# Optimization experiments

Hardware: AMD Instinct MI355X
Metric: run time of the kernel (lower is better)

## Reference

```python
import jax, jax.numpy as jnp
import numpy as np

NUM_HEADS = 16

def setup_inputs() -> dict:
    key = jax.random.key(0)
    ks = jax.random.split(key, 3)
    B, S, D = 2, 2048, 1024
    x = jax.random.normal(ks[0], (B, S, D), dtype=jnp.float32)
    # xavier-uniform style scaling for weights
    Wqkv = jax.random.normal(ks[1], (3 * D, D), dtype=jnp.float32) * (1.0 / jnp.sqrt(D))
    bqkv = jnp.zeros((3 * D,), dtype=jnp.float32)
    Wo = jax.random.normal(ks[2], (D, D), dtype=jnp.float32) * (1.0 / jnp.sqrt(D))
    bo = jnp.zeros((D,), dtype=jnp.float32)
    return {"x": x, "Wqkv": Wqkv, "bqkv": bqkv, "Wo": Wo, "bo": bo}

def reference(x, Wqkv, bqkv, Wo, bo):
    B, S, D = x.shape
    H = NUM_HEADS
    hd = D // H
    # qkv projection (torch Linear: x @ W.T + b)
    qkv = x @ Wqkv.T + bqkv                      # [B, S, 3D]
    qkv = qkv.reshape(B, S, H, 3 * hd).transpose(0, 2, 1, 3)  # [B, H, S, 3hd]
    q, k, v = jnp.split(qkv, 3, axis=-1)         # each [B, H, S, hd]
    scale = 1.0 / jnp.sqrt(jnp.asarray(hd, dtype=x.dtype))
    logits = jnp.einsum('bhqd,bhkd->bhqk', q, k) * scale  # [B, H, S, S]
    attn = jax.nn.softmax(logits, axis=-1)
    vals = jnp.einsum('bhqk,bhkd->bhqd', attn, v)         # [B, H, S, hd]
    vals = vals.transpose(0, 2, 1, 3).reshape(B, S, D)
    return vals @ Wo.T + bo
```

## Files before the change

### kernel.cpp

```cpp
#include <hip/hip_runtime.h>


typedef short short8 __attribute__((ext_vector_type(8)));
typedef unsigned short ushort8v __attribute__((ext_vector_type(8)));
typedef unsigned short ushort4v __attribute__((ext_vector_type(4)));
typedef float floatx4 __attribute__((ext_vector_type(4)));

#define S_LEN 2048
#define D_MODEL 1024
#define N_HEADS 16
#define HEAD_DIM 64

#define EXP2F(x) __builtin_amdgcn_exp2f(x)

__device__ inline float bf2f(unsigned int u16) {
    union { unsigned int i; float f; } v; v.i = u16 << 16; return v.f;
}
__device__ inline unsigned short f2b(float f) {
    union { float f; unsigned int u; } v; v.f = f;
    return (unsigned short)((v.u + 0x7FFFu + ((v.u >> 16) & 1u)) >> 16);
}
__device__ inline unsigned int fbits(float f) {
    union { float f; unsigned int u; } v; v.f = f; return v.u;
}
__device__ inline unsigned int pack_bf2(float lo, float hi) {
    return __byte_perm(fbits(lo) + 0x8000u, fbits(hi) + 0x8000u, 0x7632);
}

__device__ inline void gld_lds16(const unsigned short* g, unsigned short* lds) {
    __builtin_amdgcn_global_load_lds(
        (const __attribute__((address_space(1))) void*)g,
        (__attribute__((address_space(3))) void*)lds, 16, 0, 0);
}

__global__ __launch_bounds__(256)
void cvt3(const float* __restrict__ s0, const float* __restrict__ s1,
          const float* __restrict__ s2,
          unsigned short* __restrict__ d0, unsigned short* __restrict__ d1,
          unsigned short* __restrict__ d2,
          int n0, int n1, int n2) {
    const int total = n0 + n1 + n2;
    for (int g = blockIdx.x * blockDim.x + threadIdx.x; g < total;
         g += gridDim.x * blockDim.x) {
        const float* s; unsigned short* d; int l;
        if (g < n0)            { s = s0; d = d0; l = g; }
        else if (g < n0 + n1)  { s = s1; d = d1; l = g - n0; }
        else                   { s = s2; d = d2; l = g - n0 - n1; }
        const float4* sp = (const float4*)s + (size_t)l * 2;
        float4 f0 = sp[0], f1 = sp[1];
        ushort8v o;
        o[0] = f2b(f0.x); o[1] = f2b(f0.y); o[2] = f2b(f0.z); o[3] = f2b(f0.w);
        o[4] = f2b(f1.x); o[5] = f2b(f1.y); o[6] = f2b(f1.z); o[7] = f2b(f1.w);
        *(ushort8v*)(d + (size_t)l * 8) = o;
    }
}

__device__ inline void gemm_core(const unsigned short* __restrict__ A,
                                 const unsigned short* __restrict__ W,
                                 int m0, int n0, int K,
                                 unsigned short* As, unsigned short* Bs,
                                 floatx4 acc[4][4]) {
    const int tid  = threadIdx.x;
    const int lane = tid & 63;
    const int wave = tid >> 6;
    const int wm = wave >> 1, wn = wave & 1;
    const int r = lane & 15, q = lane >> 4;

    const int grow = wave * 32 + (lane >> 3);
    const int gcol = (lane & 7) * 8;

    for (int k0 = 0; k0 < K; k0 += 64) {
        __syncthreads();
#pragma unroll
        for (int j = 0; j < 4; j++) {
            gld_lds16(A + (size_t)(m0 + grow + j * 8) * K + k0 + gcol,
                      As + wave * 2048 + j * 512);
            gld_lds16(W + (size_t)(n0 + grow + j * 8) * K + k0 + gcol,
                      Bs + wave * 2048 + j * 512);
        }
        __builtin_amdgcn_s_waitcnt(0);
        __syncthreads();
#pragma unroll
        for (int kk = 0; kk < 64; kk += 32) {
            short8 aF[4], bF[4];
#pragma unroll
            for (int t = 0; t < 4; t++)
                aF[t] = *(const short8*)(As + (wm * 64 + t * 16 + r) * 64 + kk + q * 8);
#pragma unroll
            for (int t = 0; t < 4; t++)
                bF[t] = *(const short8*)(Bs + (wn * 64 + t * 16 + r) * 64 + kk + q * 8);
#pragma unroll
            for (int i = 0; i < 4; i++)
#pragma unroll
                for (int j = 0; j < 4; j++)
                    acc[i][j] = __builtin_amdgcn_mfma_f32_16x16x32_bf16(aF[i], bF[j], acc[i][j], 0, 0, 0);
        }
    }
}

__device__ inline void stage_h(const unsigned short* __restrict__ g, int ldk,
                               unsigned short* lds, int wave, int lane) {
    const int lr  = lane >> 3;
    const int csw = ((lane & 7) ^ lr) * 8;
    const int rw  = wave * 8 + lr;
    gld_lds16(g + (size_t)rw * ldk + csw,        lds + wave * 512);
    gld_lds16(g + (size_t)(rw + 64) * ldk + csw, lds + 4096 + wave * 512);
}

#define QLDB(pBx) do {                                                         \
    _Pragma("unroll")                                                          \
    for (int nj = 0; nj < 4; ++nj) {                                           \
        bF[nj][0] = *(const short8*)((pBx) + nj * 1024 + co0);                 \
        bF[nj][1] = *(const short8*)((pBx) + nj * 1024 + co1);                 \
    }                                                                          \
} while (0)

#define QPHASE(pAx, mq, ...) do {                                              \
    short8 aF[2][2];                                                           \
    _Pragma("unroll")                                                          \
    for (int m2 = 0; m2 < 2; ++m2) {                                           \
        aF[m2][0] = *(const short8*)((pAx) + ((mq) * 2 + m2) * 1024 + co0);    \
        aF[m2][1] = *(const short8*)((pAx) + ((mq) * 2 + m2) * 1024 + co1);    \
    }                                                                          \
    __VA_ARGS__;                                                               \
    __builtin_amdgcn_s_barrier();                                              \
    __builtin_amdgcn_s_setprio(1);                                             \
    _Pragma("unroll")                                                          \
    for (int kk = 0; kk < 2; ++kk)                                             \
        _Pragma("unroll")                                                      \
        for (int m2 = 0; m2 < 2; ++m2)                                         \
            _Pragma("unroll")                                                  \
            for (int nj = 0; nj < 4; ++nj)                                     \
                acc[(mq) * 2 + m2][nj] = __builtin_amdgcn_mfma_f32_16x16x32_bf16( \
                    aF[m2][kk], bF[nj][kk], acc[(mq) * 2 + m2][nj], 0, 0, 0);  \
    __builtin_amdgcn_s_setprio(0);                                             \
    __builtin_amdgcn_s_barrier();                                              \
} while (0)

#define WAIT_VM4() asm volatile("s_waitcnt vmcnt(4)" ::: "memory")
#define WAIT_VM0() asm volatile("s_waitcnt vmcnt(0)" ::: "memory")

__global__ __launch_bounds__(512, 2)
void qkv_gemm(const unsigned short* __restrict__ x,
              const unsigned short* __restrict__ Wqkv,
              const float* __restrict__ bqkv,
              unsigned short* __restrict__ Qb,
              unsigned short* __restrict__ Kb,
              unsigned short* __restrict__ Vb) {
    __shared__ unsigned short AS[2][16384];
    __shared__ unsigned short BS[2][16384];

    const int tid  = threadIdx.x;
    const int lane = tid & 63;
    const int wave = tid >> 6;
    const int wm = wave >> 2;
    const int wn = wave & 3;
    const int r  = lane & 15, q2 = lane >> 4;
    const int K  = D_MODEL;

    const int idx = blockIdx.x;
    const int swz = (idx & 7) * 24 + (idx >> 3);
    const int mb = swz & 15, nb = swz >> 4;
    const int m0 = mb * 256, n0 = nb * 256;

    const unsigned short* Abase = x    + (size_t)m0 * K;
    const unsigned short* Bbase = Wqkv + (size_t)n0 * K;

    const int co0 = ((q2 ^ (r & 7)) * 8);
    const int co1 = (((q2 + 4) ^ (r & 7)) * 8);
    const unsigned short* pA0 = &AS[0][(wm * 128 + r) * 64];
    const unsigned short* pA1 = &AS[1][(wm * 128 + r) * 64];
    const unsigned short* pB0 = &BS[0][(wn * 64 + r) * 64];
    const unsigned short* pB1 = &BS[1][(wn * 64 + r) * 64];

    floatx4 acc[8][4] = {};
    short8 bF[4][2];

    stage_h(Abase,                K, &AS[0][0],    wave, lane);
    stage_h(Abase + 128 * K,      K, &AS[0][8192], wave, lane);
    stage_h(Bbase,                K, &BS[0][0],    wave, lane);
    stage_h(Bbase + 128 * K,      K, &BS[0][8192], wave, lane);
    stage_h(Bbase + 64,           K, &BS[1][0],    wave, lane);
    stage_h(Bbase + 128 * K + 64, K, &BS[1][8192], wave, lane);
    WAIT_VM4();
    __builtin_amdgcn_s_barrier();

    for (int i = 0; i < 8; ++i) {
        const bool more = (i < 7);
        const int kA1 = i * 128 + 64;
        const int kT2 = i * 128 + 128;
        const int kT3 = i * 128 + 192;

        QLDB(pB0);
        QPHASE(pA0, 0, {
            stage_h(Abase + kA1,           K, &AS[1][0],    wave, lane);
            stage_h(Abase + 128 * K + kA1, K, &AS[1][8192], wave, lane);
        });
        QPHASE(pA0, 1, {
            if (more) stage_h(Bbase + kT2, K, &BS[0][0], wave, lane);
        });
        QPHASE(pA0, 2, {
            if (more) stage_h(Bbase + 128 * K + kT2, K, &BS[0][8192], wave, lane);
        });
        QPHASE(pA0, 3, {
            if (more) { WAIT_VM4(); } else { WAIT_VM0(); }
        });
        QLDB(pB1);
        QPHASE(pA1, 0, {
            if (more) {
                stage_h(Abase + kT2,           K, &AS[0][0],    wave, lane);
                stage_h(Abase + 128 * K + kT2, K, &AS[0][8192], wave, lane);
            }
        });
        QPHASE(pA1, 1, {
            if (more) stage_h(Bbase + kT3, K, &BS[1][0], wave, lane);
        });
        QPHASE(pA1, 2, {
            if (more) stage_h(Bbase + 128 * K + kT3, K, &BS[1][8192], wave, lane);
        });
        QPHASE(pA1, 3, {
            if (more) { WAIT_VM4(); }
        });
    }

#pragma unroll
    for (int mi = 0; mi < 8; mi++) {
#pragma unroll
        for (int nj = 0; nj < 4; nj++) {
            int n = n0 + wn * 64 + nj * 16 + r;
            int h = n / 192;
            int rem = n % 192;
            int typ = rem >> 6;
            int d = rem & 63;
            float bv = bqkv[n];
            int m = m0 + wm * 128 + mi * 16 + q2 * 4;
            int b = m >> 11, s = m & 2047;
            if (typ == 2) {
                ushort4v pk;
#pragma unroll
                for (int rg = 0; rg < 4; rg++) pk[rg] = f2b(acc[mi][nj][rg] + bv);
                *(ushort4v*)(Vb + ((size_t)((b * N_HEADS + h) * HEAD_DIM + d)) * S_LEN + s) = pk;
            } else {
                unsigned short* dst = (typ == 0) ? Qb : Kb;
                float sc = (typ == 0) ? 0.180336880f : 1.0f;
#pragma unroll
                for (int rg = 0; rg < 4; rg++)
                    dst[(((size_t)(b * N_HEADS + h)) * S_LEN + s + rg) * HEAD_DIM + d] =
                        f2b((acc[mi][nj][rg] + bv) * sc);
            }
        }
    }
}

__global__ __launch_bounds__(256)
void out_gemm(const unsigned short* __restrict__ vals,
              const unsigned short* __restrict__ Wo,
              const float* __restrict__ bo,
              float* __restrict__ out) {
    __shared__ unsigned short As[128 * 64];
    __shared__ unsigned short Bs[128 * 64];
    const int lane = threadIdx.x & 63;
    const int wave = threadIdx.x >> 6;
    const int wm = wave >> 1, wn = wave & 1;
    const int r = lane & 15, q = lane >> 4;
    const int m0 = blockIdx.y * 128;
    const int n0 = blockIdx.x * 128;

    floatx4 acc[4][4] = {};
    gemm_core(vals, Wo, m0, n0, D_MODEL, As, Bs, acc);

#pragma unroll
    for (int i = 0; i < 4; i++) {
#pragma unroll
        for (int j = 0; j < 4; j++) {
            int n = n0 + wn * 64 + j * 16 + r;
            float bv = bo[n];
#pragma unroll
            for (int rg = 0; rg < 4; rg++) {
                int m = m0 + wm * 64 + i * 16 + q * 4 + rg;
                out[(size_t)m * D_MODEL + n] = acc[i][j][rg] + bv;
            }
        }
    }
}

__global__ __launch_bounds__(256, 2)
void attn_kernel(const unsigned short* __restrict__ Qb,
                 const unsigned short* __restrict__ Kb,
                 const unsigned short* __restrict__ Vg,
                 unsigned short* __restrict__ vals) {
    __shared__ unsigned short QPs[128 * 64];
    __shared__ unsigned short Ks[2 * 64 * 64];
    __shared__ unsigned short Vts[2 * 64 * 64];

    const int tid = threadIdx.x;
    const int lane = tid & 63;
    const int wave = tid >> 6;
    const int r = lane & 15, q2 = lane >> 4;
    const int r7 = r & 7;
    const int w32 = wave * 32;

    const int idx  = blockIdx.x;
    const int xcd  = idx & 7;
    const int slot = idx >> 3;
    const int bh   = (xcd << 2) | (slot >> 4);
    const int q0   = (slot & 15) * 128;
    const int b = bh >> 4, h = bh & 15;

    const unsigned short* Qp = Qb + (size_t)bh * S_LEN * HEAD_DIM;
    const unsigned short* Kp = Kb + (size_t)bh * S_LEN * HEAD_DIM;
    const unsigned short* Vp = Vg + (size_t)bh * HEAD_DIM * S_LEN;

    const int srow = lane >> 3;
    const int scol = ((lane & 7) ^ srow) * 8;

    {
        const int qrow = tid >> 1;
        const int c0 = (tid & 1) * 4;
#pragma unroll
        for (int cc = 0; cc < 4; cc++) {
            int cb = c0 + cc;
            const uint4* gq = (const uint4*)(Qp + (size_t)(q0 + qrow) * HEAD_DIM + cb * 8);
            *(uint4*)(QPs + qrow * 64 + ((cb ^ (qrow & 7)) * 8)) = *gq;
        }
#pragma unroll
        for (int j = 0; j < 16; j += 8) {
            gld_lds16(Kp + (size_t)(wave * 16 + j + srow) * HEAD_DIM + scol,
                      Ks + (wave * 16 + j) * 64);
            gld_lds16(Vp + (size_t)(wave * 16 + j + srow) * S_LEN + scol,
                      Vts + (wave * 16 + j) * 64);
        }
    }
    __builtin_amdgcn_s_waitcnt(0);
    __syncthreads();

    short8 qf[2][2];
#pragma unroll
    for (int nt = 0; nt < 2; nt++)
#pragma unroll
        for (int ks = 0; ks < 2; ks++) {
            int cb = ks * 4 + q2;
            qf[nt][ks] = *(const short8*)(QPs + (w32 + nt * 16 + r) * 64 + ((cb ^ r7) * 8));
        }

    float l_part[2] = {0.f, 0.f};
    floatx4 o_acc[2][4] = {};
    int cur = 0;

    for (int kt = 0; kt < S_LEN; kt += 64) {
        const int more = (kt + 64 < S_LEN);
        if (more) {
            const int nxt = (cur ^ 1) * 4096;
#pragma unroll
            for (int j = 0; j < 16; j += 8) {
                gld_lds16(Kp + (size_t)(kt + 64 + wave * 16 + j + srow) * HEAD_DIM + scol,
                          Ks + nxt + (wave * 16 + j) * 64);
                gld_lds16(Vp + (size_t)(wave * 16 + j + srow) * S_LEN + kt + 64 + scol,
                          Vts + nxt + (wave * 16 + j) * 64);
            }
        }
        const int co = cur * 4096;

        floatx4 sp[4][2] = {};
#pragma unroll
        for (int mt = 0; mt < 4; mt++)
#pragma unroll
            for (int ks = 0; ks < 2; ks++) {
                int cb = ks * 4 + q2;
                short8 kfr = *(const short8*)(Ks + co + (mt * 16 + r) * 64 + ((cb ^ r7) * 8));
#pragma unroll
                for (int nt = 0; nt < 2; nt++)
                    sp[mt][nt] = __builtin_amdgcn_mfma_f32_16x16x32_bf16(kfr, qf[nt][ks], sp[mt][nt], 0, 0, 0);
            }

#pragma unroll
        for (int nt = 0; nt < 2; nt++)
#pragma unroll
            for (int mt = 0; mt < 4; mt++) {
#pragma unroll
                for (int reg = 0; reg < 4; reg++) {
                    float e = EXP2F(sp[mt][nt][reg]);
                    sp[mt][nt][reg] = e;
                    l_part[nt] += e;
                }
                uint2 pk;
                pk.x = pack_bf2(sp[mt][nt][0], sp[mt][nt][1]);
                pk.y = pack_bf2(sp[mt][nt][2], sp[mt][nt][3]);
                int cb = 2 * mt + (q2 >> 1);
                *(uint2*)(QPs + (w32 + nt * 16 + r) * 64 + ((cb ^ r7) * 8) + (q2 & 1) * 4) = pk;
            }

        short8 pf[2][2], vf[4][2];
#pragma unroll
        for (int nt = 0; nt < 2; nt++)
#pragma unroll
            for (int ks = 0; ks < 2; ks++) {
                int cb = ks * 4 + q2;
                pf[nt][ks] = *(const short8*)(QPs + (w32 + nt * 16 + r) * 64 + ((cb ^ r7) * 8));
            }
#pragma unroll
        for (int dt = 0; dt < 4; dt++)
#pragma unroll
            for (int ks = 0; ks < 2; ks++) {
                int cb = ks * 4 + q2;
                vf[dt][ks] = *(const short8*)(Vts + co + (dt * 16 + r) * 64 + ((cb ^ r7) * 8));
            }
#pragma unroll
        for (int nt = 0; nt < 2; nt++)
#pragma unroll
            for (int dt = 0; dt < 4; dt++)
#pragma unroll
                for (int ks = 0; ks < 2; ks++)
                    o_acc[nt][dt] = __builtin_amdgcn_mfma_f32_16x16x32_bf16(pf[nt][ks], vf[dt][ks], o_acc[nt][dt], 0, 0, 0);

        if (more) {
            __builtin_amdgcn_s_waitcnt(0);
            __syncthreads();
            cur ^= 1;
        }
    }

#pragma unroll
    for (int nt = 0; nt < 2; nt++) {
        l_part[nt] += __shfl_xor(l_part[nt], 16, 64);
        l_part[nt] += __shfl_xor(l_part[nt], 32, 64);
    }

#pragma unroll
    for (int nt = 0; nt < 2; nt++) {
#pragma unroll
        for (int reg = 0; reg < 4; reg++) {
            float inv = 1.0f / __shfl(l_part[nt], q2 * 4 + reg, 64);
            int srow2 = q0 + w32 + nt * 16 + q2 * 4 + reg;
            size_t base = ((size_t)b * S_LEN + srow2) * D_MODEL + h * HEAD_DIM + r;
#pragma unroll
            for (int dt = 0; dt < 4; dt++)
                vals[base + dt * 16] = f2b(o_acc[nt][dt][reg] * inv);
        }
    }
}

extern "C" void kernel_launch(void* const* d_in, const int* in_sizes, int n_in,
                              void* d_out, int out_size, void* d_ws, size_t ws_size,
                              hipStream_t stream) {
    const float* x    = (const float*)d_in[0];
    const float* Wqkv = (const float*)d_in[1];
    const float* bqkv = (const float*)d_in[2];
    const float* Wo   = (const float*)d_in[3];
    const float* bo   = (const float*)d_in[4];
    float* out = (float*)d_out;

    const size_t NX = 4194304, NW = 3145728, NO = 1048576;
    unsigned short* xb    = (unsigned short*)d_ws;
    unsigned short* Wqkvb = xb + NX;
    unsigned short* Wob   = Wqkvb + NW;
    unsigned short* Qb    = Wob + NO;
    unsigned short* Kb    = Qb + NX;
    unsigned short* Vb    = Kb + NX;
    unsigned short* vals  = xb;

    cvt3<<<4096, 256, 0, stream>>>(x, Wqkv, Wo, xb, Wqkvb, Wob,
                                   (int)(NX / 8), (int)(NW / 8), (int)(NO / 8));
    qkv_gemm<<<192, 512, 0, stream>>>(xb, Wqkvb, bqkv, Qb, Kb, Vb);
    attn_kernel<<<512, 256, 0, stream>>>(Qb, Kb, Vb, vals);
    out_gemm<<<dim3(8, 32), 256, 0, stream>>>(vals, Wob, bo, out);
}
```

Baseline: 196.9 us.

## Keep softmax probabilities in registers via permuted K row loading

```diff
diff --git a/kernel.cpp b/kernel.cpp
--- a/kernel.cpp
+++ b/kernel.cpp
@@ -25,6 +25,10 @@
 }
 __device__ inline unsigned int pack_bf2(float lo, float hi) {
     return __byte_perm(fbits(lo) + 0x8000u, fbits(hi) + 0x8000u, 0x7632);
+}
+
+__device__ inline int key64(int c) {
+    return (c & 0x23) | ((c & 0x0C) << 1) | ((c & 0x10) >> 2);
 }
 
 __device__ inline void gld_lds16(const unsigned short* g, unsigned short* lds) {
@@ -313,6 +317,8 @@
 
     const int srow = lane >> 3;
     const int scol = ((lane & 7) ^ srow) * 8;
+    const int kr0 = key64(wave * 16 + srow);
+    const int kr1 = key64(wave * 16 + 8 + srow);
 
     {
         const int qrow = tid >> 1;
@@ -323,13 +329,12 @@
             const uint4* gq = (const uint4*)(Qp + (size_t)(q0 + qrow) * HEAD_DIM + cb * 8);
             *(uint4*)(QPs + qrow * 64 + ((cb ^ (qrow & 7)) * 8)) = *gq;
         }
-#pragma unroll
-        for (int j = 0; j < 16; j += 8) {
-            gld_lds16(Kp + (size_t)(wave * 16 + j + srow) * HEAD_DIM + scol,
-                      Ks + (wave * 16 + j) * 64);
-            gld_lds16(Vp + (size_t)(wave * 16 + j + srow) * S_LEN + scol,
-                      Vts + (wave * 16 + j) * 64);
-        }
+        gld_lds16(Kp + (size_t)kr0 * HEAD_DIM + scol, Ks + (wave * 16) * 64);
+        gld_lds16(Kp + (size_t)kr1 * HEAD_DIM + scol, Ks + (wave * 16 + 8) * 64);
+        gld_lds16(Vp + (size_t)(wave * 16 + srow) * S_LEN + scol,
+                  Vts + (wave * 16) * 64);
+        gld_lds16(Vp + (size_t)(wave * 16 + 8 + srow) * S_LEN + scol,
+                  Vts + (wave * 16 + 8) * 64);
     }
     __builtin_amdgcn_s_waitcnt(0);
     __syncthreads();
@@ -351,17 +356,19 @@
         const int more = (kt + 64 < S_LEN);
         if (more) {
             const int nxt = (cur ^ 1) * 4096;
-#pragma unroll
-            for (int j = 0; j < 16; j += 8) {
-                gld_lds16(Kp + (size_t)(kt + 64 + wave * 16 + j + srow) * HEAD_DIM + scol,
-                          Ks + nxt + (wave * 16 + j) * 64);
-                gld_lds16(Vp + (size_t)(wave * 16 + j + srow) * S_LEN + kt + 64 + scol,
-                          Vts + nxt + (wave * 16 + j) * 64);
-            }
+            gld_lds16(Kp + (size_t)(kt + 64 + kr0) * HEAD_DIM + scol,
+                      Ks + nxt + (wave * 16) * 64);
+            gld_lds16(Kp + (size_t)(kt + 64 + kr1) * HEAD_DIM + scol,
+                      Ks + nxt + (wave * 16 + 8) * 64);
+            gld_lds16(Vp + (size_t)(wave * 16 + srow) * S_LEN + kt + 64 + scol,
+                      Vts + nxt + (wave * 16) * 64);
+            gld_lds16(Vp + (size_t)(wave * 16 + 8 + srow) * S_LEN + kt + 64 + scol,
+                      Vts + nxt + (wave * 16 + 8) * 64);
         }
         const int co = cur * 4096;
 
         floatx4 sp[4][2] = {};
+        __builtin_amdgcn_s_setprio(1);
 #pragma unroll
         for (int mt = 0; mt < 4; mt++)
 #pragma unroll
@@ -372,31 +379,30 @@
                 for (int nt = 0; nt < 2; nt++)
                     sp[mt][nt] = __builtin_amdgcn_mfma_f32_16x16x32_bf16(kfr, qf[nt][ks], sp[mt][nt], 0, 0, 0);
             }
+        __builtin_amdgcn_s_setprio(0);
 
 #pragma unroll
         for (int nt = 0; nt < 2; nt++)
 #pragma unroll
-            for (int mt = 0; mt < 4; mt++) {
+            for (int mt = 0; mt < 4; mt++)
 #pragma unroll
                 for (int reg = 0; reg < 4; reg++) {
                     float e = EXP2F(sp[mt][nt][reg]);
                     sp[mt][nt][reg] = e;
                     l_part[nt] += e;
                 }
-                uint2 pk;
-                pk.x = pack_bf2(sp[mt][nt][0], sp[mt][nt][1]);
-                pk.y = pack_bf2(sp[mt][nt][2], sp[mt][nt][3]);
-                int cb = 2 * mt + (q2 >> 1);
-                *(uint2*)(QPs + (w32 + nt * 16 + r) * 64 + ((cb ^ r7) * 8) + (q2 & 1) * 4) = pk;
-            }
-
-        short8 pf[2][2], vf[4][2];
+
+        short8 pa[2][2], vf[4][2];
 #pragma unroll
         for (int nt = 0; nt < 2; nt++)
 #pragma unroll
             for (int ks = 0; ks < 2; ks++) {
-                int cb = ks * 4 + q2;
-                pf[nt][ks] = *(const short8*)(QPs + (w32 + nt * 16 + r) * 64 + ((cb ^ r7) * 8));
+                union { unsigned int u[4]; short8 s; } t;
+                t.u[0] = pack_bf2(sp[2 * ks][nt][0],     sp[2 * ks][nt][1]);
+                t.u[1] = pack_bf2(sp[2 * ks][nt][2],     sp[2 * ks][nt][3]);
+                t.u[2] = pack_bf2(sp[2 * ks + 1][nt][0], sp[2 * ks + 1][nt][1]);
+                t.u[3] = pack_bf2(sp[2 * ks + 1][nt][2], sp[2 * ks + 1][nt][3]);
+                pa[nt][ks] = t.s;
             }
 #pragma unroll
         for (int dt = 0; dt < 4; dt++)
@@ -405,13 +411,15 @@
                 int cb = ks * 4 + q2;
                 vf[dt][ks] = *(const short8*)(Vts + co + (dt * 16 + r) * 64 + ((cb ^ r7) * 8));
             }
+        __builtin_amdgcn_s_setprio(1);
 #pragma unroll
         for (int nt = 0; nt < 2; nt++)
 #pragma unroll
             for (int dt = 0; dt < 4; dt++)
 #pragma unroll
                 for (int ks = 0; ks < 2; ks++)
-                    o_acc[nt][dt] = __builtin_amdgcn_mfma_f32_16x16x32_bf16(pf[nt][ks], vf[dt][ks], o_acc[nt][dt], 0, 0, 0);
+                    o_acc[nt][dt] = __builtin_amdgcn_mfma_f32_16x16x32_bf16(pa[nt][ks], vf[dt][ks], o_acc[nt][dt], 0, 0, 0);
+        __builtin_amdgcn_s_setprio(0);
 
         if (more) {
             __builtin_amdgcn_s_waitcnt(0);
```

Result: faster. 191.3 us (-2.9%).

## Keep P in registers, widen key tile to 128, compute row sums via MFMA

Applied to the files above, without the earlier changes.

```diff
diff --git a/kernel.cpp b/kernel.cpp
--- a/kernel.cpp
+++ b/kernel.cpp
@@ -25,6 +25,10 @@
 }
 __device__ inline unsigned int pack_bf2(float lo, float hi) {
     return __byte_perm(fbits(lo) + 0x8000u, fbits(hi) + 0x8000u, 0x7632);
+}
+
+__device__ inline int key128(int c) {
+    return (c & 0x63) | ((c & 0x0C) << 1) | ((c & 0x10) >> 2);
 }
 
 __device__ inline void gld_lds16(const unsigned short* g, unsigned short* lds) {
@@ -289,9 +293,8 @@
                  const unsigned short* __restrict__ Kb,
                  const unsigned short* __restrict__ Vg,
                  unsigned short* __restrict__ vals) {
-    __shared__ unsigned short QPs[128 * 64];
-    __shared__ unsigned short Ks[2 * 64 * 64];
-    __shared__ unsigned short Vts[2 * 64 * 64];
+    __shared__ unsigned short Ks[2 * 128 * 64];
+    __shared__ unsigned short Vts[2 * 128 * 64];
 
     const int tid = threadIdx.x;
     const int lane = tid & 63;
@@ -314,6 +317,15 @@
     const int srow = lane >> 3;
     const int scol = ((lane & 7) ^ srow) * 8;
 
+    int krow[4], vd[4], vpan[4];
+#pragma unroll
+    for (int t = 0; t < 4; t++) {
+        int c = wave * 32 + t * 8 + srow;
+        krow[t] = key128(c);
+        vpan[t] = c >> 6;
+        vd[t]   = c & 63;
+    }
+
     {
         const int qrow = tid >> 1;
         const int c0 = (tid & 1) * 4;
@@ -321,49 +333,57 @@
         for (int cc = 0; cc < 4; cc++) {
             int cb = c0 + cc;
             const uint4* gq = (const uint4*)(Qp + (size_t)(q0 + qrow) * HEAD_DIM + cb * 8);
-            *(uint4*)(QPs + qrow * 64 + ((cb ^ (qrow & 7)) * 8)) = *gq;
-        }
-#pragma unroll
-        for (int j = 0; j < 16; j += 8) {
-            gld_lds16(Kp + (size_t)(wave * 16 + j + srow) * HEAD_DIM + scol,
-                      Ks + (wave * 16 + j) * 64);
-            gld_lds16(Vp + (size_t)(wave * 16 + j + srow) * S_LEN + scol,
-                      Vts + (wave * 16 + j) * 64);
-        }
+            *(uint4*)(Ks + qrow * 64 + ((cb ^ (qrow & 7)) * 8)) = *gq;
+        }
+    }
+    __syncthreads();
+    short8 qf[2][2];
+#pragma unroll
+    for (int nt = 0; nt < 2; nt++)
+#pragma unroll
+        for (int ks = 0; ks < 2; ks++) {
+            int cb = ks * 4 + q2;
+            qf[nt][ks] = *(const short8*)(Ks + (w32 + nt * 16 + r) * 64 + ((cb ^ r7) * 8));
+        }
+    __syncthreads();
+
+#pragma unroll
+    for (int t = 0; t < 4; t++) {
+        gld_lds16(Kp + (size_t)krow[t] * HEAD_DIM + scol,
+                  Ks + (wave * 32 + t * 8) * 64);
+        gld_lds16(Vp + (size_t)vd[t] * S_LEN + vpan[t] * 64 + scol,
+                  Vts + (wave * 32 + t * 8) * 64);
     }
     __builtin_amdgcn_s_waitcnt(0);
     __syncthreads();
 
-    short8 qf[2][2];
-#pragma unroll
-    for (int nt = 0; nt < 2; nt++)
-#pragma unroll
-        for (int ks = 0; ks < 2; ks++) {
-            int cb = ks * 4 + q2;
-            qf[nt][ks] = *(const short8*)(QPs + (w32 + nt * 16 + r) * 64 + ((cb ^ r7) * 8));
-        }
-
-    float l_part[2] = {0.f, 0.f};
+    union { unsigned int u[4]; short8 s; } onesu;
+    onesu.u[0] = 0x3F803F80u; onesu.u[1] = 0x3F803F80u;
+    onesu.u[2] = 0x3F803F80u; onesu.u[3] = 0x3F803F80u;
+    const short8 onesf = onesu.s;
+
+    floatx4 l_acc[2] = {};
     floatx4 o_acc[2][4] = {};
     int cur = 0;
 
-    for (int kt = 0; kt < S_LEN; kt += 64) {
-        const int more = (kt + 64 < S_LEN);
+    for (int kt = 0; kt < S_LEN; kt += 128) {
+        const int more = (kt + 128 < S_LEN);
         if (more) {
-            const int nxt = (cur ^ 1) * 4096;
-#pragma unroll
-            for (int j = 0; j < 16; j += 8) {
-                gld_lds16(Kp + (size_t)(kt + 64 + wave * 16 + j + srow) * HEAD_DIM + scol,
-                          Ks + nxt + (wave * 16 + j) * 64);
-                gld_lds16(Vp + (size_t)(wave * 16 + j + srow) * S_LEN + kt + 64 + scol,
-                          Vts + nxt + (wave * 16 + j) * 64);
-            }
-        }
-        const int co = cur * 4096;
-
-        floatx4 sp[4][2] = {};
-#pragma unroll
-        for (int mt = 0; mt < 4; mt++)
+            const int nxt = (cur ^ 1) * 8192;
+#pragma unroll
+            for (int t = 0; t < 4; t++) {
+                gld_lds16(Kp + (size_t)(kt + 128 + krow[t]) * HEAD_DIM + scol,
+                          Ks + nxt + (wave * 32 + t * 8) * 64);
+                gld_lds16(Vp + (size_t)vd[t] * S_LEN + kt + 128 + vpan[t] * 64 + scol,
+                          Vts + nxt + (wave * 32 + t * 8) * 64);
+            }
+        }
+        const int co = cur * 8192;
+
+        floatx4 sp[8][2] = {};
+        __builtin_amdgcn_s_setprio(1);
+#pragma unroll
+        for (int mt = 0; mt < 8; mt++)
 #pragma unroll
             for (int ks = 0; ks < 2; ks++) {
                 int cb = ks * 4 + q2;
@@ -372,46 +392,50 @@
                 for (int nt = 0; nt < 2; nt++)
                     sp[mt][nt] = __builtin_amdgcn_mfma_f32_16x16x32_bf16(kfr, qf[nt][ks], sp[mt][nt], 0, 0, 0);
             }
+        __builtin_amdgcn_s_setprio(0);
 
 #pragma unroll
         for (int nt = 0; nt < 2; nt++)
 #pragma unroll
-            for (int mt = 0; mt < 4; mt++) {
-#pragma unroll
-                for (int reg = 0; reg < 4; reg++) {
-                    float e = EXP2F(sp[mt][nt][reg]);
-                    sp[mt][nt][reg] = e;
-                    l_part[nt] += e;
-                }
-                uint2 pk;
-                pk.x = pack_bf2(sp[mt][nt][0], sp[mt][nt][1]);
-                pk.y = pack_bf2(sp[mt][nt][2], sp[mt][nt][3]);
-                int cb = 2 * mt + (q2 >> 1);
-                *(uint2*)(QPs + (w32 + nt * 16 + r) * 64 + ((cb ^ r7) * 8) + (q2 & 1) * 4) = pk;
-            }
-
-        short8 pf[2][2], vf[4][2];
+            for (int mt = 0; mt < 8; mt++)
+#pragma unroll
+                for (int reg = 0; reg < 4; reg++)
+                    sp[mt][nt][reg] = EXP2F(sp[mt][nt][reg]);
+
+        short8 pa[2][4];
 #pragma unroll
         for (int nt = 0; nt < 2; nt++)
 #pragma unroll
-            for (int ks = 0; ks < 2; ks++) {
-                int cb = ks * 4 + q2;
-                pf[nt][ks] = *(const short8*)(QPs + (w32 + nt * 16 + r) * 64 + ((cb ^ r7) * 8));
-            }
-#pragma unroll
-        for (int dt = 0; dt < 4; dt++)
-#pragma unroll
-            for (int ks = 0; ks < 2; ks++) {
-                int cb = ks * 4 + q2;
-                vf[dt][ks] = *(const short8*)(Vts + co + (dt * 16 + r) * 64 + ((cb ^ r7) * 8));
-            }
+            for (int ks = 0; ks < 4; ks++) {
+                union { unsigned int u[4]; short8 s; } tw;
+                tw.u[0] = pack_bf2(sp[2 * ks][nt][0],     sp[2 * ks][nt][1]);
+                tw.u[1] = pack_bf2(sp[2 * ks][nt][2],     sp[2 * ks][nt][3]);
+                tw.u[2] = pack_bf2(sp[2 * ks + 1][nt][0], sp[2 * ks + 1][nt][1]);
+                tw.u[3] = pack_bf2(sp[2 * ks + 1][nt][2], sp[2 * ks + 1][nt][3]);
+                pa[nt][ks] = tw.s;
+            }
+
+        __builtin_amdgcn_s_setprio(1);
+#pragma unroll
+        for (int dt = 0; dt < 4; dt++) {
+            short8 vf[4];
+#pragma unroll
+            for (int ks = 0; ks < 4; ks++) {
+                int cb = (ks & 1) * 4 + q2;
+                vf[ks] = *(const short8*)(Vts + co + (ks >> 1) * 4096 + (dt * 16 + r) * 64 + ((cb ^ r7) * 8));
+            }
+#pragma unroll
+            for (int nt = 0; nt < 2; nt++)
+#pragma unroll
+                for (int ks = 0; ks < 4; ks++)
+                    o_acc[nt][dt] = __builtin_amdgcn_mfma_f32_16x16x32_bf16(pa[nt][ks], vf[ks], o_acc[nt][dt], 0, 0, 0);
+        }
 #pragma unroll
         for (int nt = 0; nt < 2; nt++)
 #pragma unroll
-            for (int dt = 0; dt < 4; dt++)
-#pragma unroll
-                for (int ks = 0; ks < 2; ks++)
-                    o_acc[nt][dt] = __builtin_amdgcn_mfma_f32_16x16x32_bf16(pf[nt][ks], vf[dt][ks], o_acc[nt][dt], 0, 0, 0);
+            for (int ks = 0; ks < 4; ks++)
+                l_acc[nt] = __builtin_amdgcn_mfma_f32_16x16x32_bf16(pa[nt][ks], onesf, l_acc[nt], 0, 0, 0);
+        __builtin_amdgcn_s_setprio(0);
 
         if (more) {
             __builtin_amdgcn_s_waitcnt(0);
@@ -422,15 +446,9 @@
 
 #pragma unroll
     for (int nt = 0; nt < 2; nt++) {
-        l_part[nt] += __shfl_xor(l_part[nt], 16, 64);
-        l_part[nt] += __shfl_xor(l_part[nt], 32, 64);
-    }
-
-#pragma unroll
-    for (int nt = 0; nt < 2; nt++) {
 #pragma unroll
         for (int reg = 0; reg < 4; reg++) {
-            float inv = 1.0f / __shfl(l_part[nt], q2 * 4 + reg, 64);
+            float inv = 1.0f / l_acc[nt][reg];
             int srow2 = q0 + w32 + nt * 16 + q2 * 4 + reg;
             size_t base = ((size_t)b * S_LEN + srow2) * D_MODEL + h * HEAD_DIM + r;
 #pragma unroll
```

After: 184.6 us. 6.2% less time.
